# Performance work log

Hardware: AMD Instinct MI355X
Metric: run time of the kernel (lower is better)

The kernel has to match this reference:

```python
import jax, jax.numpy as jnp
import numpy as np
import math

D_MODEL = 512
H = 8
N_LAYERS = 4
D_FF = 2048
HEAD_DIM = D_MODEL // H


def setup_inputs() -> dict:
    key = jax.random.key(0)
    ks = jax.random.split(key, 12)
    s = 1.0 / math.sqrt(D_MODEL)
    x = jax.random.normal(ks[0], (16, 1024, D_MODEL), dtype=jnp.float32)
    # shared head module (same weights for all H heads, per original ModuleList aliasing)
    wq = jax.random.normal(ks[1], (D_MODEL, HEAD_DIM), dtype=jnp.float32) * s
    bq = jnp.zeros((HEAD_DIM,), dtype=jnp.float32)
    wk = jax.random.normal(ks[2], (D_MODEL, HEAD_DIM), dtype=jnp.float32) * s
    bk = jnp.zeros((HEAD_DIM,), dtype=jnp.float32)
    wv = jax.random.normal(ks[3], (D_MODEL, HEAD_DIM), dtype=jnp.float32) * s
    bv = jnp.zeros((HEAD_DIM,), dtype=jnp.float32)
    wo = jax.random.normal(ks[4], (D_MODEL, D_MODEL), dtype=jnp.float32) * s
    bo = jnp.zeros((D_MODEL,), dtype=jnp.float32)
    # shared LayerNorm params (one LN instance used everywhere)
    ln_g = jnp.ones((D_MODEL,), dtype=jnp.float32)
    ln_b = jnp.zeros((D_MODEL,), dtype=jnp.float32)
    w1 = jax.random.normal(ks[5], (D_MODEL, D_FF), dtype=jnp.float32) * s
    b1 = jnp.zeros((D_FF,), dtype=jnp.float32)
    w2 = jax.random.normal(ks[6], (D_FF, D_MODEL), dtype=jnp.float32) * (1.0 / math.sqrt(D_FF))
    b2 = jnp.zeros((D_MODEL,), dtype=jnp.float32)
    return {"x": x, "wq": wq, "bq": bq, "wk": wk, "bk": bk, "wv": wv, "bv": bv,
            "wo": wo, "bo": bo, "ln_g": ln_g, "ln_b": ln_b,
            "w1": w1, "b1": b1, "w2": w2, "b2": b2}


def _layernorm(x, g, b, eps=1e-5):
    mu = jnp.mean(x, axis=-1, keepdims=True)
    var = jnp.var(x, axis=-1, keepdims=True)
    return (x - mu) * jax.lax.rsqrt(var + eps) * g + b


def _mha(x, wq, bq, wk, bk, wv, bv, wo, bo):
    # All H heads share identical weights, so compute one head and tile the concat.
    q = x @ wq + bq                      # [b, s, hd]
    k = x @ wk + bk                      # [b, s, hd]
    v = x @ wv + bv                      # [b, s, hd]
    scores = jnp.einsum('bqd,bkd->bqk', q, k) / math.sqrt(D_MODEL / H)
    # NOTE: original applies Softmax(dim=1) on a [b, s_q, s_k] tensor -> softmax over q axis
    attn = jax.nn.softmax(scores, axis=1)
    head = jnp.einsum('bqk,bkd->bqd', attn, v)   # [b, s, hd]
    concat = jnp.tile(head, (1, 1, H))           # [b, s, d_model] (H identical heads)
    return concat @ wo + bo


def reference(x, wq, bq, wk, bk, wv, bv, wo, bo, ln_g, ln_b, w1, b1, w2, b2):
    for _ in range(N_LAYERS):
        attn = _mha(x, wq, bq, wk, bk, wv, bv, wo, bo)
        h = _layernorm(attn + x, ln_g, ln_b)
        ff = (jnp.maximum(h @ w1 + b1, 0.0) if False else (h @ w1 + b1)) @ w2 + b2  # no relu in original forward
        x = _layernorm(h + ff, ln_g, ln_b)
    return x
```

## Files before the change

### kernel.cpp

```cpp
#include <hip/hip_runtime.h>
#include <hip/hip_bf16.h>

#define DEV __device__ __forceinline__

typedef __bf16 bf16;
typedef __attribute__((ext_vector_type(8))) __bf16 bf16x8;
typedef __attribute__((ext_vector_type(4))) __bf16 bf16x4;
typedef __attribute__((ext_vector_type(4))) float f32x4;

static constexpr int B = 16, S = 1024, D = 512, HD = 64, FF = 2048;
static constexpr int BS = B * S;
static constexpr int QKVLD = 192;

typedef const __attribute__((address_space(1))) void gas_void;
typedef __attribute__((address_space(3))) void las_void;

DEV void gload16(const void* g, void* l) {
  __builtin_amdgcn_global_load_lds((gas_void*)g, (las_void*)l, 16, 0, 0);
}

DEV void store_out(float* p, float v) { *p = v; }
DEV void store_out(bf16* p, float v) { *p = (bf16)v; }

template<int BM, int BN, int BK, int WM, int WN, typename OutT>
__global__ __launch_bounds__(WM* WN * 64) void k_gemm(
    const bf16* __restrict__ A, const bf16* __restrict__ Bt, OutT* __restrict__ C,
    int K, int lda, int ldb, int ldc, float alpha, const float* __restrict__ bias,
    long aB, long bB, long cB)
{
  constexpr int NW = WM * WN;
  constexpr int T = NW * 64;
  constexpr int FM = BM / WM / 16;
  constexpr int FN = BN / WN / 16;
  constexpr int CPR = BK / 8;
  constexpr int CHA = BM * BK / 8;
  constexpr int CHB = BN * BK / 8;
  constexpr int IA = CHA / T;
  constexpr int IB = CHB / T;
  static_assert(CHA % T == 0 && CHB % T == 0, "staging divisibility");

  __shared__ bf16 sA[BM * BK];
  __shared__ bf16 sB[BN * BK];

  const int tid = threadIdx.x;
  const int lane = tid & 63;
  const int wid = tid >> 6;
  const int wm = wid / WN, wn = wid % WN;
  const int bm0 = blockIdx.x * BM;
  const int bn0 = blockIdx.y * BN;
  A += (long)blockIdx.z * aB + (long)bm0 * lda;
  Bt += (long)blockIdx.z * bB + (long)bn0 * ldb;
  C += (long)blockIdx.z * cB;

  f32x4 acc[FM][FN] = {};

  const int lr = lane & 15;
  const int lk = (lane >> 4) * 8;

  for (int k0 = 0; k0 < K; k0 += BK) {
#pragma unroll
    for (int i = 0; i < IA; ++i) {
      int c = i * T + tid;
      int row = c / CPR, kc = (c % CPR) * 8;
      gload16(A + (long)row * lda + k0 + kc, sA + c * 8);
    }
#pragma unroll
    for (int i = 0; i < IB; ++i) {
      int c = i * T + tid;
      int row = c / CPR, kc = (c % CPR) * 8;
      gload16(Bt + (long)row * ldb + k0 + kc, sB + c * 8);
    }
    asm volatile("s_waitcnt vmcnt(0)" ::: "memory");
    __syncthreads();

#pragma unroll
    for (int kk = 0; kk < BK; kk += 32) {
      bf16x8 af[FM], bg[FN];
#pragma unroll
      for (int m = 0; m < FM; ++m) {
        int row = wm * (FM * 16) + m * 16 + lr;
        af[m] = *(const bf16x8*)(sA + row * BK + kk + lk);
      }
#pragma unroll
      for (int n = 0; n < FN; ++n) {
        int col = wn * (FN * 16) + n * 16 + lr;
        bg[n] = *(const bf16x8*)(sB + col * BK + kk + lk);
      }
#pragma unroll
      for (int m = 0; m < FM; ++m)
#pragma unroll
        for (int n = 0; n < FN; ++n)
          acc[m][n] = __builtin_amdgcn_mfma_f32_16x16x32_bf16(af[m], bg[n], acc[m][n], 0, 0, 0);
    }
    __syncthreads();
  }

  const int r0 = (lane >> 4) * 4;
#pragma unroll
  for (int m = 0; m < FM; ++m) {
#pragma unroll
    for (int n = 0; n < FN; ++n) {
      int col = bn0 + wn * (FN * 16) + n * 16 + lr;
      float bv = bias ? bias[col] : 0.f;
#pragma unroll
      for (int r = 0; r < 4; ++r) {
        int row = bm0 + wm * (FM * 16) + m * 16 + r0 + r;
        store_out(C + (long)row * ldc + col, acc[m][n][r] * alpha + bv);
      }
    }
  }
}

__global__ __launch_bounds__(256) void k_cvt_dual(const float* __restrict__ in,
    float* __restrict__ fo, bf16* __restrict__ bo, long n4)
{
  long i = (long)blockIdx.x * 256 + threadIdx.x;
  if (i >= n4) return;
  float4 v = ((const float4*)in)[i];
  ((float4*)fo)[i] = v;
  bf16x4 h; h[0] = (bf16)v.x; h[1] = (bf16)v.y; h[2] = (bf16)v.z; h[3] = (bf16)v.w;
  ((bf16x4*)bo)[i] = h;
}

__global__ void k_tr(const float* __restrict__ in, bf16* __restrict__ out, int R, int C)
{
  __shared__ float t[32][33];
  int c0 = blockIdx.x * 32, r0 = blockIdx.y * 32;
#pragma unroll
  for (int i = 0; i < 4; ++i) {
    int r = r0 + threadIdx.y + i * 8;
    t[threadIdx.y + i * 8][threadIdx.x] = in[(long)r * C + c0 + threadIdx.x];
  }
  __syncthreads();
#pragma unroll
  for (int i = 0; i < 4; ++i) {
    int c = c0 + threadIdx.y + i * 8;
    out[(long)c * R + r0 + threadIdx.x] = (bf16)t[threadIdx.x][threadIdx.y + i * 8];
  }
}

__global__ __launch_bounds__(256) void k_woe(const float* __restrict__ wo, bf16* __restrict__ woet)
{
  int idx = blockIdx.x * 256 + threadIdx.x;
  int j = idx & 511, d = idx >> 9;
  float s = 0.f;
#pragma unroll
  for (int h = 0; h < 8; ++h) s += wo[(long)(h * 64 + d) * 512 + j];
  woet[(long)j * 64 + d] = (bf16)s;
}

__global__ void k_pack_bias(const float* __restrict__ bq, const float* __restrict__ bk,
                            const float* __restrict__ bv, float* __restrict__ o)
{
  int t = threadIdx.x;
  o[t] = bq[t]; o[64 + t] = bk[t]; o[128 + t] = bv[t];
}

__global__ __launch_bounds__(256) void k_exp(bf16* __restrict__ p, long n8)
{
  long i = (long)blockIdx.x * 256 + threadIdx.x;
  if (i >= n8) return;
  bf16x8 v = ((bf16x8*)p)[i];
#pragma unroll
  for (int j = 0; j < 8; ++j) v[j] = (bf16)__expf((float)v[j]);
  ((bf16x8*)p)[i] = v;
}

__global__ __launch_bounds__(256) void k_colsum(const bf16* __restrict__ P, float* __restrict__ cs)
{
  int k = blockIdx.x * 256 + threadIdx.x;
  int b = blockIdx.y;
  const bf16* p = P + (long)b * S * S + k;
  float a0 = 0, a1 = 0, a2 = 0, a3 = 0;
  for (int q = 0; q < S; q += 4) {
    a0 += (float)p[(long)q * S];
    a1 += (float)p[(long)(q + 1) * S];
    a2 += (float)p[(long)(q + 2) * S];
    a3 += (float)p[(long)(q + 3) * S];
  }
  cs[b * S + k] = (a0 + a1) + (a2 + a3);
}

__global__ __launch_bounds__(256) void k_build_vnt(const bf16* __restrict__ qkv,
    const float* __restrict__ cs, bf16* __restrict__ vnt)
{
  int d = threadIdx.x & 63;
  int k = blockIdx.x * 4 + (threadIdx.x >> 6);
  int b = blockIdx.y;
  float v = (float)qkv[((long)(b * S + k)) * QKVLD + 128 + d];
  vnt[((long)b * HD + d) * S + k] = (bf16)(v / cs[b * S + k]);
}

__global__ __launch_bounds__(256) void k_add_ln(const float* __restrict__ a,
    const float* __restrict__ b, const float* __restrict__ g, const float* __restrict__ be,
    float* __restrict__ fo, bf16* __restrict__ bo)
{
  int row = blockIdx.x * 4 + (threadIdx.x >> 6);
  int lane = threadIdx.x & 63;
  const float4* pa = (const float4*)(a + (long)row * D);
  const float4* pb = (const float4*)(b + (long)row * D);
  float4 v[2];
  float s = 0.f, s2 = 0.f;
#pragma unroll
  for (int j = 0; j < 2; ++j) {
    float4 x = pa[lane + j * 64];
    float4 y = pb[lane + j * 64];
    float4 t;
    t.x = x.x + y.x; t.y = x.y + y.y; t.z = x.z + y.z; t.w = x.w + y.w;
    v[j] = t;
    s += t.x + t.y + t.z + t.w;
    s2 += t.x * t.x + t.y * t.y + t.z * t.z + t.w * t.w;
  }
#pragma unroll
  for (int o = 32; o > 0; o >>= 1) { s += __shfl_xor(s, o); s2 += __shfl_xor(s2, o); }
  float mean = s * (1.f / D);
  float var = s2 * (1.f / D) - mean * mean;
  float rstd = rsqrtf(var + 1e-5f);
#pragma unroll
  for (int j = 0; j < 2; ++j) {
    int ci = lane + j * 64;
    float4 gv = ((const float4*)g)[ci];
    float4 bv = ((const float4*)be)[ci];
    float4 t = v[j], y;
    y.x = (t.x - mean) * rstd * gv.x + bv.x;
    y.y = (t.y - mean) * rstd * gv.y + bv.y;
    y.z = (t.z - mean) * rstd * gv.z + bv.z;
    y.w = (t.w - mean) * rstd * gv.w + bv.w;
    ((float4*)(fo + (long)row * D))[ci] = y;
    bf16x4 h; h[0] = (bf16)y.x; h[1] = (bf16)y.y; h[2] = (bf16)y.z; h[3] = (bf16)y.w;
    *(bf16x4*)(bo + (long)row * D + ci * 4) = h;
  }
}

extern "C" void kernel_launch(void* const* d_in, const int* in_sizes, int n_in,
                              void* d_out, int out_size, void* d_ws, size_t ws_size,
                              hipStream_t stream) {
  const float* x_in = (const float*)d_in[0];
  const float* wq = (const float*)d_in[1];
  const float* bq = (const float*)d_in[2];
  const float* wk = (const float*)d_in[3];
  const float* bk = (const float*)d_in[4];
  const float* wv = (const float*)d_in[5];
  const float* bv = (const float*)d_in[6];
  const float* wo = (const float*)d_in[7];
  const float* bo = (const float*)d_in[8];
  const float* ln_g = (const float*)d_in[9];
  const float* ln_b = (const float*)d_in[10];
  const float* w1 = (const float*)d_in[11];
  const float* b1 = (const float*)d_in[12];
  const float* w2 = (const float*)d_in[13];
  const float* b2 = (const float*)d_in[14];
  float* f_x = (float*)d_out;

  char* w = (char*)d_ws;
  size_t off = 0;
  auto alloc = [&](size_t bytes) { void* p = w + off; off += (bytes + 255) & ~(size_t)255; return p; };
  float* f_tmp = (float*)alloc((size_t)BS * D * 4);
  float* f_h   = (float*)alloc((size_t)BS * D * 4);
  bf16* b_x    = (bf16*)alloc((size_t)BS * D * 2);
  bf16* b_h    = (bf16*)alloc((size_t)BS * D * 2);
  bf16* b_qkv  = (bf16*)alloc((size_t)BS * QKVLD * 2);
  bf16* b_big  = (bf16*)alloc((size_t)BS * FF * 2);
  float* f_cs  = (float*)alloc((size_t)B * S * 4);
  bf16* b_vnt  = (bf16*)alloc((size_t)B * HD * S * 2);
  bf16* b_head = (bf16*)alloc((size_t)BS * HD * 2);
  bf16* wqkvT  = (bf16*)alloc((size_t)QKVLD * D * 2);
  bf16* woeT   = (bf16*)alloc((size_t)D * HD * 2);
  bf16* w1T    = (bf16*)alloc((size_t)FF * D * 2);
  bf16* w2T    = (bf16*)alloc((size_t)D * FF * 2);
  float* f_bqkv = (float*)alloc(192 * 4);

  k_cvt_dual<<<dim3(BS * D / 4 / 256), 256, 0, stream>>>(x_in, f_x, b_x, (long)BS * D / 4);
  k_tr<<<dim3(HD / 32, D / 32), dim3(32, 8), 0, stream>>>(wq, wqkvT, D, HD);
  k_tr<<<dim3(HD / 32, D / 32), dim3(32, 8), 0, stream>>>(wk, wqkvT + 64 * D, D, HD);
  k_tr<<<dim3(HD / 32, D / 32), dim3(32, 8), 0, stream>>>(wv, wqkvT + 128 * D, D, HD);
  k_tr<<<dim3(FF / 32, D / 32), dim3(32, 8), 0, stream>>>(w1, w1T, D, FF);
  k_tr<<<dim3(D / 32, FF / 32), dim3(32, 8), 0, stream>>>(w2, w2T, FF, D);
  k_woe<<<dim3(128), 256, 0, stream>>>(wo, woeT);
  k_pack_bias<<<1, 64, 0, stream>>>(bq, bk, bv, f_bqkv);

  for (int layer = 0; layer < 4; ++layer) {
    k_gemm<128, 64, 64, 4, 1, bf16><<<dim3(BS / 128, 3, 1), 256, 0, stream>>>(
        b_x, wqkvT, b_qkv, D, D, D, QKVLD, 1.f, f_bqkv, 0, 0, 0);
    k_gemm<128, 128, 64, 2, 2, bf16><<<dim3(S / 128, S / 128, B), 256, 0, stream>>>(
        b_qkv, b_qkv + 64, b_big, HD, QKVLD, QKVLD, S, 0.125f, nullptr,
        (long)S * QKVLD, (long)S * QKVLD, (long)S * S);
    k_exp<<<dim3((int)((long)B * S * S / 8 / 256)), 256, 0, stream>>>(b_big, (long)B * S * S / 8);
    k_colsum<<<dim3(S / 256, B), 256, 0, stream>>>(b_big, f_cs);
    k_build_vnt<<<dim3(S / 4, B), 256, 0, stream>>>(b_qkv, f_cs, b_vnt);
    k_gemm<128, 64, 64, 4, 1, bf16><<<dim3(S / 128, 1, B), 256, 0, stream>>>(
        b_big, b_vnt, b_head, S, S, S, HD, 1.f, nullptr,
        (long)S * S, (long)HD * S, (long)S * HD);
    k_gemm<128, 128, 64, 2, 2, float><<<dim3(BS / 128, D / 128, 1), 256, 0, stream>>>(
        b_head, woeT, f_tmp, HD, HD, HD, D, 1.f, bo, 0, 0, 0);
    k_add_ln<<<dim3(BS / 4), 256, 0, stream>>>(f_tmp, f_x, ln_g, ln_b, f_h, b_h);
    k_gemm<128, 128, 64, 2, 2, bf16><<<dim3(BS / 128, FF / 128, 1), 256, 0, stream>>>(
        b_h, w1T, b_big, D, D, D, FF, 1.f, b1, 0, 0, 0);
    k_gemm<128, 128, 64, 2, 2, float><<<dim3(BS / 128, D / 128, 1), 256, 0, stream>>>(
        b_big, w2T, f_tmp, FF, FF, FF, D, 1.f, b2, 0, 0, 0);
    k_add_ln<<<dim3(BS / 4), 256, 0, stream>>>(f_tmp, f_h, ln_g, ln_b, f_x, b_x);
  }
}
```

Baseline: 1.147 ms.

## Add pipelined 8-wave GEMM for FFN, fuse exp into score GEMM epilogue

```diff
diff --git a/kernel.cpp b/kernel.cpp
--- a/kernel.cpp
+++ b/kernel.cpp
@@ -22,7 +22,139 @@
 DEV void store_out(float* p, float v) { *p = v; }
 DEV void store_out(bf16* p, float v) { *p = (bf16)v; }
 
-template<int BM, int BN, int BK, int WM, int WN, typename OutT>
+#define MEMFENCE asm volatile("" ::: "memory")
+#define VMCNT(n) asm volatile("s_waitcnt vmcnt(" #n ")" ::: "memory")
+
+template<int BM, typename OutT>
+__global__ __launch_bounds__(512, 1) void k_gemm8p(
+    const bf16* __restrict__ A, const bf16* __restrict__ Bt, OutT* __restrict__ C,
+    int K, int lda, int ldb, int ldc, int gn, float alpha, const float* __restrict__ bias)
+{
+  static_assert(BM == 128 || BM == 256, "");
+  constexpr int HM = BM / 2;
+  constexpr int FMH = HM / 2 / 16;
+  constexpr int GL_A = HM / 64;
+  constexpr int GL_B = 2;
+
+  __shared__ bf16 sA[2][2][HM * 64];
+  __shared__ bf16 sB[2][2][128 * 64];
+
+  const int tid = threadIdx.x;
+  const int lane = tid & 63;
+  const int wid = tid >> 6;
+  const int wm = wid >> 2;
+  const int wn = wid & 3;
+  const int lr = lane & 15;
+  const int lk8 = (lane >> 4) * 8;
+
+  const int nwg = gridDim.x;
+  const int bid = blockIdx.x;
+  const int swz = (bid & 7) * (nwg >> 3) + (bid >> 3);
+  const int im = swz / gn, in = swz % gn;
+  const int bm0 = im * BM, bn0 = in * 256;
+
+  A += (long)bm0 * lda;
+  Bt += (long)bn0 * ldb;
+
+  const int NT = K >> 6;
+  const int NI = NT >> 1;
+
+  auto stageA = [&](int buf, int h, int t) {
+    if (t >= NT) return;
+    const bf16* src = A + (long)t * 64;
+#pragma unroll
+    for (int it = 0; it < GL_A; ++it) {
+      int c = it * 512 + tid;
+      int row = c >> 3;
+      int cc = (c & 7) ^ (row & 7);
+      gload16(src + (long)(h * HM + row) * lda + cc * 8, &sA[buf][h][c * 8]);
+    }
+  };
+  auto stageB = [&](int buf, int h, int t) {
+    if (t >= NT) return;
+    const bf16* src = Bt + (long)t * 64;
+#pragma unroll
+    for (int it = 0; it < GL_B; ++it) {
+      int c = it * 512 + tid;
+      int row = c >> 3;
+      int cc = (c & 7) ^ (row & 7);
+      gload16(src + (long)(h * 128 + row) * ldb + cc * 8, &sB[buf][h][c * 8]);
+    }
+  };
+
+  f32x4 acc[4][FMH * 2] = {};
+
+  stageA(0, 0, 0); stageB(0, 1, 0); stageA(0, 1, 0); stageB(0, 0, 0);
+  stageA(1, 0, 1); stageB(1, 1, 1);
+  if (GL_A == 2) { VMCNT(4); } else { VMCNT(3); }
+  MEMFENCE; __builtin_amdgcn_s_barrier(); MEMFENCE;
+
+#define PHASE(b, qm, qn, STAGE, ...) do {                                        \
+    bf16x8 af[FMH][2], bg[2][2];                                                 \
+    _Pragma("unroll") for (int fm = 0; fm < FMH; ++fm)                           \
+    _Pragma("unroll") for (int kx = 0; kx < 2; ++kx) {                           \
+      int ra = wm * (HM / 2) + fm * 16 + lr;                                     \
+      int e = kx * 32 + lk8;                                                     \
+      af[fm][kx] = *(const bf16x8*)((const char*)&sA[b][qm][0] +                 \
+                     (ra * 8 + ((e >> 3) ^ (ra & 7))) * 16);                     \
+    }                                                                            \
+    _Pragma("unroll") for (int fn = 0; fn < 2; ++fn)                             \
+    _Pragma("unroll") for (int kx = 0; kx < 2; ++kx) {                           \
+      int rb = wn * 32 + fn * 16 + lr;                                           \
+      int e = kx * 32 + lk8;                                                     \
+      bg[fn][kx] = *(const bf16x8*)((const char*)&sB[b][qn][0] +                 \
+                     (rb * 8 + ((e >> 3) ^ (rb & 7))) * 16);                     \
+    }                                                                            \
+    STAGE;                                                                       \
+    MEMFENCE; __builtin_amdgcn_s_barrier(); MEMFENCE;                            \
+    __builtin_amdgcn_s_setprio(1);                                               \
+    _Pragma("unroll") for (int kx = 0; kx < 2; ++kx)                             \
+    _Pragma("unroll") for (int fm = 0; fm < FMH; ++fm)                           \
+    _Pragma("unroll") for (int fn = 0; fn < 2; ++fn)                             \
+      acc[qm * 2 + qn][fm * 2 + fn] = __builtin_amdgcn_mfma_f32_16x16x32_bf16(   \
+          af[fm][kx], bg[fn][kx], acc[qm * 2 + qn][fm * 2 + fn], 0, 0, 0);       \
+    __builtin_amdgcn_s_setprio(0);                                               \
+    __VA_ARGS__;                                                                 \
+    MEMFENCE; __builtin_amdgcn_s_barrier(); MEMFENCE;                            \
+  } while (0)
+
+  for (int i = 0; i < NI; ++i) {
+    const int t1 = 2 * i + 1, t2 = 2 * i + 2, t3 = 2 * i + 3;
+    const bool more = (t2 < NT);
+    PHASE(0, 0, 0, stageA(1, 1, t1));
+    PHASE(0, 0, 1, stageB(1, 0, t1));
+    PHASE(0, 1, 1, stageA(0, 0, t2));
+    PHASE(0, 1, 0, stageB(0, 1, t2),
+          if (more) { if (GL_A == 2) { VMCNT(4); } else { VMCNT(3); } }
+          else { VMCNT(0); });
+    PHASE(1, 0, 0, stageA(0, 1, t2));
+    PHASE(1, 0, 1, stageB(0, 0, t2));
+    PHASE(1, 1, 1, stageA(1, 0, t3));
+    PHASE(1, 1, 0, stageB(1, 1, t3),
+          if (more) { if (GL_A == 2) { VMCNT(4); } else { VMCNT(3); } });
+  }
+#undef PHASE
+
+  const int r0 = (lane >> 4) * 4;
+#pragma unroll
+  for (int qm = 0; qm < 2; ++qm)
+#pragma unroll
+  for (int qn = 0; qn < 2; ++qn)
+#pragma unroll
+  for (int fm = 0; fm < FMH; ++fm)
+#pragma unroll
+  for (int fn = 0; fn < 2; ++fn) {
+    int gc = bn0 + qn * 128 + wn * 32 + fn * 16 + lr;
+    float bv = bias ? bias[gc] : 0.f;
+#pragma unroll
+    for (int r = 0; r < 4; ++r) {
+      int gr = bm0 + qm * HM + wm * (HM / 2) + fm * 16 + r0 + r;
+      store_out(C + (long)gr * ldc + gc, acc[qm * 2 + qn][fm * 2 + fn][r] * alpha + bv);
+    }
+  }
+}
+
+template<int BM, int BN, int BK, int WM, int WN, typename OutT, bool EXPF>
 __global__ __launch_bounds__(WM* WN * 64) void k_gemm(
     const bf16* __restrict__ A, const bf16* __restrict__ Bt, OutT* __restrict__ C,
     int K, int lda, int ldb, int ldc, float alpha, const float* __restrict__ bias,
@@ -53,7 +185,6 @@
   C += (long)blockIdx.z * cB;
 
   f32x4 acc[FM][FN] = {};
-
   const int lr = lane & 15;
   const int lk = (lane >> 4) * 8;
 
@@ -105,7 +236,9 @@
 #pragma unroll
       for (int r = 0; r < 4; ++r) {
         int row = bm0 + wm * (FM * 16) + m * 16 + r0 + r;
-        store_out(C + (long)row * ldc + col, acc[m][n][r] * alpha + bv);
+        float v = acc[m][n][r] * alpha + bv;
+        if (EXPF) v = __expf(v);
+        store_out(C + (long)row * ldc + col, v);
       }
     }
   }
@@ -154,16 +287,6 @@
 {
   int t = threadIdx.x;
   o[t] = bq[t]; o[64 + t] = bk[t]; o[128 + t] = bv[t];
-}
-
-__global__ __launch_bounds__(256) void k_exp(bf16* __restrict__ p, long n8)
-{
-  long i = (long)blockIdx.x * 256 + threadIdx.x;
-  if (i >= n8) return;
-  bf16x8 v = ((bf16x8*)p)[i];
-#pragma unroll
-  for (int j = 0; j < 8; ++j) v[j] = (bf16)__expf((float)v[j]);
-  ((bf16x8*)p)[i] = v;
 }
 
 __global__ __launch_bounds__(256) void k_colsum(const bf16* __restrict__ P, float* __restrict__ cs)
@@ -280,24 +403,23 @@
   k_pack_bias<<<1, 64, 0, stream>>>(bq, bk, bv, f_bqkv);
 
   for (int layer = 0; layer < 4; ++layer) {
-    k_gemm<128, 64, 64, 4, 1, bf16><<<dim3(BS / 128, 3, 1), 256, 0, stream>>>(
+    k_gemm<128, 64, 64, 4, 1, bf16, false><<<dim3(BS / 128, 3, 1), 256, 0, stream>>>(
         b_x, wqkvT, b_qkv, D, D, D, QKVLD, 1.f, f_bqkv, 0, 0, 0);
-    k_gemm<128, 128, 64, 2, 2, bf16><<<dim3(S / 128, S / 128, B), 256, 0, stream>>>(
+    k_gemm<128, 128, 64, 2, 2, bf16, true><<<dim3(S / 128, S / 128, B), 256, 0, stream>>>(
         b_qkv, b_qkv + 64, b_big, HD, QKVLD, QKVLD, S, 0.125f, nullptr,
         (long)S * QKVLD, (long)S * QKVLD, (long)S * S);
-    k_exp<<<dim3((int)((long)B * S * S / 8 / 256)), 256, 0, stream>>>(b_big, (long)B * S * S / 8);
     k_colsum<<<dim3(S / 256, B), 256, 0, stream>>>(b_big, f_cs);
     k_build_vnt<<<dim3(S / 4, B), 256, 0, stream>>>(b_qkv, f_cs, b_vnt);
-    k_gemm<128, 64, 64, 4, 1, bf16><<<dim3(S / 128, 1, B), 256, 0, stream>>>(
+    k_gemm<64, 64, 64, 4, 1, bf16, false><<<dim3(S / 64, 1, B), 256, 0, stream>>>(
         b_big, b_vnt, b_head, S, S, S, HD, 1.f, nullptr,
         (long)S * S, (long)HD * S, (long)S * HD);
-    k_gemm<128, 128, 64, 2, 2, float><<<dim3(BS / 128, D / 128, 1), 256, 0, stream>>>(
+    k_gemm<128, 128, 64, 2, 2, float, false><<<dim3(BS / 128, D / 128, 1), 256, 0, stream>>>(
         b_head, woeT, f_tmp, HD, HD, HD, D, 1.f, bo, 0, 0, 0);
     k_add_ln<<<dim3(BS / 4), 256, 0, stream>>>(f_tmp, f_x, ln_g, ln_b, f_h, b_h);
-    k_gemm<128, 128, 64, 2, 2, bf16><<<dim3(BS / 128, FF / 128, 1), 256, 0, stream>>>(
-        b_h, w1T, b_big, D, D, D, FF, 1.f, b1, 0, 0, 0);
-    k_gemm<128, 128, 64, 2, 2, float><<<dim3(BS / 128, D / 128, 1), 256, 0, stream>>>(
-        b_big, w2T, f_tmp, FF, FF, FF, D, 1.f, b2, 0, 0, 0);
+    k_gemm8p<256, bf16><<<dim3((BS / 256) * (FF / 256)), 512, 0, stream>>>(
+        b_h, w1T, b_big, D, D, D, FF, FF / 256, 1.f, b1);
+    k_gemm8p<128, float><<<dim3((BS / 128) * (D / 256)), 512, 0, stream>>>(
+        b_big, w2T, f_tmp, FF, FF, FF, D, D / 256, 1.f, b2);
     k_add_ln<<<dim3(BS / 4), 256, 0, stream>>>(f_tmp, f_h, ln_g, ln_b, f_x, b_x);
   }
 }
```

New measurement: 1.018 ms. 1.13x faster.
